# Kernel tuning notes

Measured on AMD Instinct MI355X. Metric: run time of the kernel, lower is better.

The kernel has to match this reference:

```python
import jax, jax.numpy as jnp
import numpy as np

N_NODES = 50000
N_EDGES = 400000
DIMS = [512, 512, 512, 512]  # input + 3 hidden
NUM_CLASSES = 40


def setup_inputs() -> dict:
    key = jax.random.key(0)
    ks = jax.random.split(key, 16)
    feat = jax.random.normal(ks[0], (N_NODES, DIMS[0]), dtype=jnp.float32)
    src = jax.random.randint(ks[1], (N_EDGES,), 0, N_NODES, dtype=jnp.int32)
    dst = jax.random.randint(ks[2], (N_EDGES,), 0, N_NODES, dtype=jnp.int32)
    params = {}
    for i in range(3):
        fan_in = DIMS[i]
        s = 1.0 / np.sqrt(fan_in)
        params[f"W{i}"] = jax.random.uniform(ks[3 + 2 * i], (DIMS[i], DIMS[i + 1]), jnp.float32, -s, s)
        params[f"b{i}"] = jax.random.uniform(ks[4 + 2 * i], (DIMS[i + 1],), jnp.float32, -s, s)
    s = 1.0 / np.sqrt(DIMS[-1])
    params["Wc"] = jax.random.uniform(ks[10], (DIMS[-1], NUM_CLASSES), jnp.float32, -s, s)
    params["bc"] = jax.random.uniform(ks[11], (NUM_CLASSES,), jnp.float32, -s, s)
    return {"feat": feat, "src": src, "dst": dst, **params}


def _gin_layer(h, src, dst, W, b):
    # DGL GINConv, aggregator='sum', eps=0: rst = (1+eps)*h + sum_{j in N(i)} h_j
    agg = jax.ops.segment_sum(h[src], dst, num_segments=N_NODES)  # [N, D]
    return jax.nn.relu((h + agg) @ W + b)  # apply_func Linear, then relu (dropout p=0)


def reference(feat, src, dst, W0, b0, W1, b1, W2, b2, Wc, bc):
    h = _gin_layer(feat, src, dst, W0, b0)
    h = _gin_layer(h, src, dst, W1, b1)
    h = _gin_layer(h, src, dst, W2, b2)
    return h @ Wc + bc  # [N, num_classes]
```

## Files before the change

kernel.cpp:

```cpp
#include <hip/hip_runtime.h>

#define N_NODES 50000
#define N_EDGES 400000
#define D 512
#define NCLS 40
#define SCAN_BLOCKS ((N_NODES + 255) / 256)
#define CSTRIDE 260

typedef __attribute__((ext_vector_type(8))) __bf16 bf16x8;
typedef __attribute__((ext_vector_type(4))) float f32x4;
typedef __attribute__((ext_vector_type(4))) float float4v;
typedef __attribute__((ext_vector_type(8))) unsigned short ushort8v;
typedef __attribute__((ext_vector_type(4))) unsigned short ushort4v;

#define AS1 __attribute__((address_space(1)))
#define AS3 __attribute__((address_space(3)))

__device__ __forceinline__ float bf2f(unsigned short u) {
  union { unsigned int i; float f; } v; v.i = ((unsigned int)u) << 16; return v.f;
}
__device__ __forceinline__ unsigned short f2bf(float f) {
  union { float f; unsigned int i; } v; v.f = f;
  unsigned int u = v.i;
  u += 0x7fffu + ((u >> 16) & 1u);
  return (unsigned short)(u >> 16);
}

__global__ void hist_kernel(const int* __restrict__ dst, int* __restrict__ counts) {
  int e = blockIdx.x * blockDim.x + threadIdx.x;
  if (e < N_EDGES) atomicAdd(&counts[dst[e]], 1);
}

__global__ __launch_bounds__(256) void scan_local_kernel(const int* __restrict__ counts,
    int* __restrict__ incl, int* __restrict__ bsum) {
  __shared__ int s[256];
  int i = blockIdx.x * 256 + threadIdx.x;
  int v = (i < N_NODES) ? counts[i] : 0;
  s[threadIdx.x] = v;
  __syncthreads();
#pragma unroll
  for (int o = 1; o < 256; o <<= 1) {
    int t = (threadIdx.x >= o) ? s[threadIdx.x - o] : 0;
    __syncthreads();
    s[threadIdx.x] += t;
    __syncthreads();
  }
  if (i < N_NODES) incl[i] = s[threadIdx.x];
  if (threadIdx.x == 255) bsum[blockIdx.x] = s[255];
}

__global__ __launch_bounds__(256) void scan_bsum_kernel(int* __restrict__ bsum) {
  __shared__ int s[256];
  int v = (threadIdx.x < SCAN_BLOCKS) ? bsum[threadIdx.x] : 0;
  s[threadIdx.x] = v;
  __syncthreads();
#pragma unroll
  for (int o = 1; o < 256; o <<= 1) {
    int t = (threadIdx.x >= o) ? s[threadIdx.x - o] : 0;
    __syncthreads();
    s[threadIdx.x] += t;
    __syncthreads();
  }
  if (threadIdx.x < SCAN_BLOCKS) bsum[threadIdx.x] = s[threadIdx.x] - v;
}

__global__ __launch_bounds__(256) void scan_finish_kernel(const int* __restrict__ counts,
    const int* __restrict__ bsum, int* __restrict__ row_ptr, int* __restrict__ cursor) {
  int i = blockIdx.x * 256 + threadIdx.x;
  if (i < N_NODES) {
    int inc = cursor[i] + bsum[blockIdx.x];
    row_ptr[i + 1] = inc;
    cursor[i] = inc - counts[i];
    if (i == 0) row_ptr[0] = 0;
  }
}

__global__ void fill_kernel(const int* __restrict__ src, const int* __restrict__ dst,
                            int* __restrict__ cursor, int* __restrict__ esrc) {
  int e = blockIdx.x * blockDim.x + threadIdx.x;
  if (e < N_EDGES) {
    int pos = atomicAdd(&cursor[dst[e]], 1);
    esrc[pos] = src[e];
  }
}

__global__ void cvt_feat_kernel(const float* __restrict__ feat, unsigned short* __restrict__ hb) {
  size_t i = (size_t)(blockIdx.x * blockDim.x + threadIdx.x) * 4;
  if (i < (size_t)N_NODES * D) {
    float4v v = *(const float4v*)&feat[i];
    ushort4v o;
    o[0] = f2bf(v[0]); o[1] = f2bf(v[1]); o[2] = f2bf(v[2]); o[3] = f2bf(v[3]);
    *(ushort4v*)&hb[i] = o;
  }
}

__global__ void cvt_w_all_kernel(const float* __restrict__ W0, const float* __restrict__ W1,
                                 const float* __restrict__ W2, const float* __restrict__ Wc,
                                 unsigned short* __restrict__ Wt, unsigned short* __restrict__ Wct) {
  int i = blockIdx.x * blockDim.x + threadIdx.x;
  if (i < 3 * D * D) {
    int l = i >> 18;
    int r = i & (D * D - 1);
    int n = r >> 9, k = r & 511;
    const float* W = (l == 0) ? W0 : ((l == 1) ? W1 : W2);
    Wt[i] = f2bf(W[k * D + n]);
  } else {
    int r = i - 3 * D * D;
    if (r < 48 * D) {
      int n = r >> 9, k = r & 511;
      Wct[r] = (n < NCLS) ? f2bf(Wc[k * NCLS + n]) : (unsigned short)0;
    }
  }
}

__global__ __launch_bounds__(256) void agg_kernel(const unsigned short* __restrict__ hb,
    const int* __restrict__ row_ptr, const int* __restrict__ esrc,
    unsigned short* __restrict__ zb) {
  int w = threadIdx.x >> 6, lane = threadIdx.x & 63;
  int node = blockIdx.x * 4 + w;
  int col = lane * 8;
  const unsigned short* hcol = hb + col;
  float acc[8];
  ushort8v v = *(const ushort8v*)&hcol[(size_t)node * D];
#pragma unroll
  for (int t = 0; t < 8; ++t) acc[t] = bf2f(v[t]);
  int s = row_ptr[node], e = row_ptr[node + 1];
  int j = s;
  for (; j + 4 <= e; j += 4) {
    int i0 = esrc[j + 0], i1 = esrc[j + 1], i2 = esrc[j + 2], i3 = esrc[j + 3];
    ushort8v v0 = *(const ushort8v*)&hcol[(size_t)i0 * D];
    ushort8v v1 = *(const ushort8v*)&hcol[(size_t)i1 * D];
    ushort8v v2 = *(const ushort8v*)&hcol[(size_t)i2 * D];
    ushort8v v3 = *(const ushort8v*)&hcol[(size_t)i3 * D];
#pragma unroll
    for (int t = 0; t < 8; ++t) acc[t] += bf2f(v0[t]);
#pragma unroll
    for (int t = 0; t < 8; ++t) acc[t] += bf2f(v1[t]);
#pragma unroll
    for (int t = 0; t < 8; ++t) acc[t] += bf2f(v2[t]);
#pragma unroll
    for (int t = 0; t < 8; ++t) acc[t] += bf2f(v3[t]);
  }
  for (; j < e; ++j) {
    int sn = esrc[j];
    ushort8v nv = *(const ushort8v*)&hcol[(size_t)sn * D];
#pragma unroll
    for (int t = 0; t < 8; ++t) acc[t] += bf2f(nv[t]);
  }
  ushort8v o;
#pragma unroll
  for (int t = 0; t < 8; ++t) o[t] = f2bf(acc[t]);
  *(ushort8v*)&zb[(size_t)node * D + col] = o;
}

__global__ __launch_bounds__(512, 4) void gemm_kernel(
    const unsigned short* __restrict__ Z, const unsigned short* __restrict__ Wt,
    const float* __restrict__ bias, unsigned short* __restrict__ Hout, int M) {
  __shared__ unsigned short smem[128 * CSTRIDE];
  unsigned short* As = smem;
  const int tid = threadIdx.x;
  const int lane = tid & 63;
  const int w = tid >> 6;
  const int wm = (w >> 2) * 64;
  const int wn = (w & 3) * 64;
  const int quad = lane >> 4;
  const int r16 = lane & 15;

  const int nwg = gridDim.x * gridDim.y;
  const int lin = blockIdx.y * gridDim.x + blockIdx.x;
  const int q = nwg >> 3, r = nwg & 7;
  const int xcd = lin & 7, idx = lin >> 3;
  const int wg = (xcd < r ? xcd * (q + 1) : r * (q + 1) + (xcd - r) * q) + idx;
  const int n0 = (wg & 1) * 256;
  const int m0 = (wg >> 1) * 128;

  f32x4 acc[4][4];
#pragma unroll
  for (int i = 0; i < 4; ++i)
#pragma unroll
    for (int j = 0; j < 4; ++j)
      acc[i][j] = (f32x4){0.f, 0.f, 0.f, 0.f};

  const int srow = lane >> 2;
  const int skk = (lane & 3) * 8;
  int gm_st = m0 + w * 16 + srow; if (gm_st > M - 1) gm_st = M - 1;
  const unsigned short* Zst = Z + (size_t)gm_st * D + skk;
  const unsigned short* Wb = Wt + (size_t)(n0 + wn + r16) * D + quad * 8;

  __builtin_amdgcn_global_load_lds((AS1 void*)(void*)Zst,
                                   (AS3 void*)(As + w * 512), 16, 0, 0);
  int cur = 0;
  for (int kt = 0; kt < 16; ++kt) {
    __syncthreads();
    if (kt < 15)
      __builtin_amdgcn_global_load_lds((AS1 void*)(void*)(Zst + (kt + 1) * 32),
                                       (AS3 void*)(As + (cur ^ 1) * 4096 + w * 512), 16, 0, 0);
    const unsigned short* Ac = As + cur * 4096;
    bf16x8 a[4];
#pragma unroll
    for (int i = 0; i < 4; ++i)
      a[i] = *(const bf16x8*)&Ac[(wm + i * 16 + r16) * 32 + quad * 8];
    const int kk = kt * 32;
#pragma unroll
    for (int j = 0; j < 4; ++j) {
      bf16x8 b = *(const bf16x8*)&Wb[(size_t)j * 16 * D + kk];
#pragma unroll
      for (int i = 0; i < 4; ++i)
        acc[i][j] = __builtin_amdgcn_mfma_f32_16x16x32_bf16(a[i], b, acc[i][j], 0, 0, 0);
    }
    cur ^= 1;
  }

  __syncthreads();
  unsigned short* Cs = smem;
#pragma unroll
  for (int j = 0; j < 4; ++j) {
    float bv = bias[n0 + wn + j * 16 + r16];
#pragma unroll
    for (int i = 0; i < 4; ++i) {
      int crow = wm + i * 16 + quad * 4;
      int ccol = wn + j * 16 + r16;
#pragma unroll
      for (int rr = 0; rr < 4; ++rr) {
        float vv = acc[i][j][rr] + bv;
        vv = vv > 0.f ? vv : 0.f;
        Cs[(crow + rr) * CSTRIDE + ccol] = f2bf(vv);
      }
    }
  }
  __syncthreads();
#pragma unroll
  for (int it = 0; it < 8; ++it) {
    int row = it * 16 + (tid >> 5);
    int colofs = (tid & 31) * 8;
    int gm = m0 + row;
    if (gm < M) {
      ushort8v vv = *(const ushort8v*)&Cs[row * CSTRIDE + colofs];
      *(ushort8v*)&Hout[(size_t)gm * D + n0 + colofs] = vv;
    }
  }
}

__global__ __launch_bounds__(256) void cls_kernel(const unsigned short* __restrict__ hb,
    const unsigned short* __restrict__ Wct, const float* __restrict__ bc,
    float* __restrict__ out) {
  int w = threadIdx.x >> 6, lane = threadIdx.x & 63;
  int quad = lane >> 4, r16 = lane & 15;
  int nb = blockIdx.x * 64 + w * 16;
  int arow = nb + r16; if (arow > N_NODES - 1) arow = N_NODES - 1;
  f32x4 acc[3];
#pragma unroll
  for (int j = 0; j < 3; ++j) acc[j] = (f32x4){0.f, 0.f, 0.f, 0.f};
#pragma unroll 4
  for (int kt = 0; kt < 16; ++kt) {
    int kk = kt * 32 + quad * 8;
    bf16x8 a = *(const bf16x8*)&hb[(size_t)arow * D + kk];
#pragma unroll
    for (int j = 0; j < 3; ++j) {
      bf16x8 b = *(const bf16x8*)&Wct[(size_t)(j * 16 + r16) * D + kk];
      acc[j] = __builtin_amdgcn_mfma_f32_16x16x32_bf16(a, b, acc[j], 0, 0, 0);
    }
  }
#pragma unroll
  for (int j = 0; j < 3; ++j) {
    int gn = j * 16 + r16;
    if (gn < NCLS) {
      float bv = bc[gn];
#pragma unroll
      for (int r = 0; r < 4; ++r) {
        int gm = nb + quad * 4 + r;
        if (gm < N_NODES) out[(size_t)gm * NCLS + gn] = acc[j][r] + bv;
      }
    }
  }
}

extern "C" void kernel_launch(void* const* d_in, const int* in_sizes, int n_in,
                              void* d_out, int out_size, void* d_ws, size_t ws_size,
                              hipStream_t stream) {
  const float* feat = (const float*)d_in[0];
  const int* src = (const int*)d_in[1];
  const int* dst = (const int*)d_in[2];
  const float* W0 = (const float*)d_in[3];
  const float* b0 = (const float*)d_in[4];
  const float* W1 = (const float*)d_in[5];
  const float* b1 = (const float*)d_in[6];
  const float* W2 = (const float*)d_in[7];
  const float* b2 = (const float*)d_in[8];
  const float* Wc = (const float*)d_in[9];
  const float* bc = (const float*)d_in[10];
  float* out = (float*)d_out;

  char* ws = (char*)d_ws;
  size_t off = 0;
  auto alloc = [&](size_t bytes) {
    char* p = ws + off;
    off += (bytes + 255) & ~(size_t)255;
    return p;
  };
  unsigned short* hb = (unsigned short*)alloc((size_t)N_NODES * D * 2);
  unsigned short* zb = (unsigned short*)alloc((size_t)N_NODES * D * 2);
  unsigned short* Wt = (unsigned short*)alloc((size_t)3 * D * D * 2);
  unsigned short* Wct = (unsigned short*)alloc((size_t)48 * D * 2);
  int* row_ptr = (int*)alloc((size_t)(N_NODES + 1) * 4);
  int* counts  = (int*)alloc((size_t)N_NODES * 4);
  int* cursor  = (int*)alloc((size_t)N_NODES * 4);
  int* esrc    = (int*)alloc((size_t)N_EDGES * 4);
  int* bsum    = (int*)alloc((size_t)256 * 4);

  hipMemsetAsync(counts, 0, (size_t)N_NODES * 4, stream);
  hist_kernel<<<(N_EDGES + 255) / 256, 256, 0, stream>>>(dst, counts);
  scan_local_kernel<<<SCAN_BLOCKS, 256, 0, stream>>>(counts, cursor, bsum);
  scan_bsum_kernel<<<1, 256, 0, stream>>>(bsum);
  scan_finish_kernel<<<SCAN_BLOCKS, 256, 0, stream>>>(counts, bsum, row_ptr, cursor);
  fill_kernel<<<(N_EDGES + 255) / 256, 256, 0, stream>>>(src, dst, cursor, esrc);

  cvt_feat_kernel<<<(N_NODES * D / 4 + 255) / 256, 256, 0, stream>>>(feat, hb);
  cvt_w_all_kernel<<<(3 * D * D + 48 * D + 255) / 256, 256, 0, stream>>>(W0, W1, W2, Wc, Wt, Wct);

  dim3 ggrid(2, (N_NODES + 127) / 128);
  const float* bs[3] = {b0, b1, b2};
  for (int l = 0; l < 3; ++l) {
    agg_kernel<<<N_NODES / 4, 256, 0, stream>>>(hb, row_ptr, esrc, zb);
    gemm_kernel<<<ggrid, 512, 0, stream>>>(zb, Wt + (size_t)l * D * D, bs[l], hb, N_NODES);
  }
  cls_kernel<<<(N_NODES + 63) / 64, 256, 0, stream>>>(hb, Wct, bc, out);
}
```

Before: 682.8 us.

## Deepen GEMM prefetch with triple-buffered LDS and register double-buffered weights

The GEMM main loop now keeps three LDS buffers for the activation tile, so the global-to-LDS copy runs two K-steps ahead. The weight fragments are loaded one step early into a double-buffered register array. Explicit vmcnt waits and a raw s_barrier, with sched_barriers around them, replace __syncthreads, and the loop is fully unrolled. The aim is to hide global load latency behind the MFMAs, at the cost of more LDS, more registers and fragile hand-placed wait counts.

```diff
diff --git a/kernel.cpp b/kernel.cpp
--- a/kernel.cpp
+++ b/kernel.cpp
@@ -187,28 +187,48 @@
   const unsigned short* Zst = Z + (size_t)gm_st * D + skk;
   const unsigned short* Wb = Wt + (size_t)(n0 + wn + r16) * D + quad * 8;
 
+  bf16x8 breg[2][4];
+
   __builtin_amdgcn_global_load_lds((AS1 void*)(void*)Zst,
                                    (AS3 void*)(As + w * 512), 16, 0, 0);
-  int cur = 0;
+  __builtin_amdgcn_sched_barrier(0);
+#pragma unroll
+  for (int j = 0; j < 4; ++j)
+    breg[0][j] = *(const bf16x8*)&Wb[(size_t)j * 16 * D];
+  __builtin_amdgcn_sched_barrier(0);
+  __builtin_amdgcn_global_load_lds((AS1 void*)(void*)(Zst + 32),
+                                   (AS3 void*)(As + 4096 + w * 512), 16, 0, 0);
+  __builtin_amdgcn_sched_barrier(0);
+
+#pragma unroll
   for (int kt = 0; kt < 16; ++kt) {
-    __syncthreads();
-    if (kt < 15)
-      __builtin_amdgcn_global_load_lds((AS1 void*)(void*)(Zst + (kt + 1) * 32),
-                                       (AS3 void*)(As + (cur ^ 1) * 4096 + w * 512), 16, 0, 0);
-    const unsigned short* Ac = As + cur * 4096;
+    if (kt == 15) asm volatile("s_waitcnt vmcnt(0)" ::: "memory");
+    else          asm volatile("s_waitcnt vmcnt(1)" ::: "memory");
+    __builtin_amdgcn_sched_barrier(0);
+    __builtin_amdgcn_s_barrier();
+    __builtin_amdgcn_sched_barrier(0);
+    if (kt + 1 < 16) {
+#pragma unroll
+      for (int j = 0; j < 4; ++j)
+        breg[(kt + 1) & 1][j] = *(const bf16x8*)&Wb[(size_t)j * 16 * D + (kt + 1) * 32];
+      __builtin_amdgcn_sched_barrier(0);
+    }
+    if (kt + 2 < 16) {
+      __builtin_amdgcn_global_load_lds((AS1 void*)(void*)(Zst + (kt + 2) * 32),
+          (AS3 void*)(As + ((kt + 2) % 3) * 4096 + w * 512), 16, 0, 0);
+      __builtin_amdgcn_sched_barrier(0);
+    }
+    const unsigned short* Ac = As + (kt % 3) * 4096;
     bf16x8 a[4];
 #pragma unroll
     for (int i = 0; i < 4; ++i)
       a[i] = *(const bf16x8*)&Ac[(wm + i * 16 + r16) * 32 + quad * 8];
-    const int kk = kt * 32;
 #pragma unroll
     for (int j = 0; j < 4; ++j) {
-      bf16x8 b = *(const bf16x8*)&Wb[(size_t)j * 16 * D + kk];
 #pragma unroll
       for (int i = 0; i < 4; ++i)
-        acc[i][j] = __builtin_amdgcn_mfma_f32_16x16x32_bf16(a[i], b, acc[i][j], 0, 0, 0);
-    }
-    cur ^= 1;
+        acc[i][j] = __builtin_amdgcn_mfma_f32_16x16x32_bf16(a[i], breg[kt & 1][j], acc[i][j], 0, 0, 0);
+    }
   }
 
   __syncthreads();
```

New measurement: 681.2 us. Within noise of the previous version (-0.2%).

## Stage weight tiles through LDS with triple-buffered async pipeline in GEMM

Applied to the files above, without the earlier changes.

The GEMM kernel now copies both the activation tile and the weight tile into LDS using direct global-to-LDS loads, instead of reading weights straight from global memory inside the MFMA loop. A three-slot ring buffer keeps two stages of loads in flight, controlled by explicit vmcnt waits and raw barriers. The aim is to hide global-load latency and stop every wave from fetching weight rows redundantly. In exchange the kernel uses more LDS per block (about 72KB), which may reduce occupancy. It also depends on hand-written waitcnt values matching the number of outstanding loads.

```diff
diff --git a/kernel.cpp b/kernel.cpp
--- a/kernel.cpp
+++ b/kernel.cpp
@@ -6,6 +6,7 @@
 #define NCLS 40
 #define SCAN_BLOCKS ((N_NODES + 255) / 256)
 #define CSTRIDE 260
+#define SLOT 12288
 
 typedef __attribute__((ext_vector_type(8))) __bf16 bf16x8;
 typedef __attribute__((ext_vector_type(4))) float f32x4;
@@ -156,8 +157,7 @@
 __global__ __launch_bounds__(512, 4) void gemm_kernel(
     const unsigned short* __restrict__ Z, const unsigned short* __restrict__ Wt,
     const float* __restrict__ bias, unsigned short* __restrict__ Hout, int M) {
-  __shared__ unsigned short smem[128 * CSTRIDE];
-  unsigned short* As = smem;
+  __shared__ unsigned short smem[3 * SLOT];
   const int tid = threadIdx.x;
   const int lane = tid & 63;
   const int w = tid >> 6;
@@ -185,30 +185,46 @@
   const int skk = (lane & 3) * 8;
   int gm_st = m0 + w * 16 + srow; if (gm_st > M - 1) gm_st = M - 1;
   const unsigned short* Zst = Z + (size_t)gm_st * D + skk;
-  const unsigned short* Wb = Wt + (size_t)(n0 + wn + r16) * D + quad * 8;
-
-  __builtin_amdgcn_global_load_lds((AS1 void*)(void*)Zst,
-                                   (AS3 void*)(As + w * 512), 16, 0, 0);
-  int cur = 0;
+  const unsigned short* Bst0 = Wt + (size_t)(n0 + w * 32 + srow) * D + skk;
+  const unsigned short* Bst1 = Wt + (size_t)(n0 + w * 32 + 16 + srow) * D + skk;
+
+  auto stage = [&](int kt_, unsigned short* p) {
+    __builtin_amdgcn_global_load_lds((AS1 void*)(void*)(Zst + kt_ * 32),
+                                     (AS3 void*)(p + w * 512), 16, 0, 0);
+    __builtin_amdgcn_global_load_lds((AS1 void*)(void*)(Bst0 + kt_ * 32),
+                                     (AS3 void*)(p + 4096 + (w * 2 + 0) * 512), 16, 0, 0);
+    __builtin_amdgcn_global_load_lds((AS1 void*)(void*)(Bst1 + kt_ * 32),
+                                     (AS3 void*)(p + 4096 + (w * 2 + 1) * 512), 16, 0, 0);
+  };
+
+  unsigned short* p0 = smem;
+  unsigned short* p1 = smem + SLOT;
+  unsigned short* p2 = smem + 2 * SLOT;
+
+  stage(0, p0);
+  stage(1, p1);
+
   for (int kt = 0; kt < 16; ++kt) {
-    __syncthreads();
-    if (kt < 15)
-      __builtin_amdgcn_global_load_lds((AS1 void*)(void*)(Zst + (kt + 1) * 32),
-                                       (AS3 void*)(As + (cur ^ 1) * 4096 + w * 512), 16, 0, 0);
-    const unsigned short* Ac = As + cur * 4096;
+    if (kt < 15) asm volatile("s_waitcnt vmcnt(3)" ::: "memory");
+    else         asm volatile("s_waitcnt vmcnt(0)" ::: "memory");
+    __builtin_amdgcn_s_barrier();
+    __builtin_amdgcn_sched_barrier(0);
+    if (kt + 2 < 16) stage(kt + 2, p2);
+    __builtin_amdgcn_sched_barrier(0);
+    const unsigned short* Ac = p0;
+    const unsigned short* Bc = p0 + 4096;
     bf16x8 a[4];
 #pragma unroll
     for (int i = 0; i < 4; ++i)
       a[i] = *(const bf16x8*)&Ac[(wm + i * 16 + r16) * 32 + quad * 8];
-    const int kk = kt * 32;
 #pragma unroll
     for (int j = 0; j < 4; ++j) {
-      bf16x8 b = *(const bf16x8*)&Wb[(size_t)j * 16 * D + kk];
+      bf16x8 b = *(const bf16x8*)&Bc[(wn + j * 16 + r16) * 32 + quad * 8];
 #pragma unroll
       for (int i = 0; i < 4; ++i)
         acc[i][j] = __builtin_amdgcn_mfma_f32_16x16x32_bf16(a[i], b, acc[i][j], 0, 0, 0);
     }
-    cur ^= 1;
+    unsigned short* t = p0; p0 = p1; p1 = p2; p2 = t;
   }
 
   __syncthreads();
```

Measured after the change: 579.1 us. -15.2%, faster.
